# Kernel optimization log

Hardware: AMD Instinct MI355X
Metric: run time of the kernel (lower is better)

## Reference

```python
import jax, jax.numpy as jnp
import numpy as np

D = 8
W = 256
NUM_FREQS = 10
NUM_FREQS_VIEWS = 4
SKIPS = (4,)
PE_DIM = 3 + 2 * 3 * NUM_FREQS        # 63
VE_DIM = 3 + 2 * 3 * NUM_FREQS_VIEWS  # 27
N_RAYS, N_SAMPLES = 4096, 64


def embed(x, num_freqs):
    # torch order: [x, sin(x*f0), cos(x*f0), sin(x*f1), cos(x*f1), ...]
    freqs = (2.0 ** jnp.arange(num_freqs)).astype(x.dtype)
    xf = x[..., None, :] * freqs[:, None]              # [..., F, 3]
    sc = jnp.stack([jnp.sin(xf), jnp.cos(xf)], axis=-2)  # [..., F, 2, 3]
    return jnp.concatenate([x, sc.reshape(*x.shape[:-1], num_freqs * 6)], -1)


def setup_inputs() -> dict:
    key = jax.random.key(0)
    ks = iter(jax.random.split(key, 32))
    inp = {}
    inp["input_pts"] = jax.random.normal(next(ks), (N_RAYS, N_SAMPLES, 3), jnp.float32)
    inp["input_views"] = jax.random.normal(next(ks), (N_RAYS, 3), jnp.float32)
    # pts MLP: layer 5 (index 5) takes W + PE_DIM due to skip after layer 4
    in_dims = [PE_DIM] + [(W + PE_DIM) if i in SKIPS else W for i in range(D - 1)]
    for i, d in enumerate(in_dims):
        inp[f"pts_w{i}"] = jax.random.normal(next(ks), (d, W), jnp.float32) / np.sqrt(d).astype(np.float32)
        inp[f"pts_b{i}"] = jnp.zeros((W,), jnp.float32)
    inp["views_w"] = jax.random.normal(next(ks), (VE_DIM + W, W // 2), jnp.float32) / np.sqrt(VE_DIM + W).astype(np.float32)
    inp["views_b"] = jnp.zeros((W // 2,), jnp.float32)
    inp["feat_w"] = jax.random.normal(next(ks), (W, W), jnp.float32) / np.sqrt(W).astype(np.float32)
    inp["feat_b"] = jnp.zeros((W,), jnp.float32)
    inp["alpha_w"] = jax.random.normal(next(ks), (W, 1), jnp.float32) / np.sqrt(W).astype(np.float32)
    inp["alpha_b"] = jnp.zeros((1,), jnp.float32)
    inp["rgb_w"] = jax.random.normal(next(ks), (W // 2, 3), jnp.float32) / np.sqrt(W // 2).astype(np.float32)
    inp["rgb_b"] = jnp.zeros((3,), jnp.float32)
    return inp


def reference(input_pts, input_views,
              pts_w0, pts_b0, pts_w1, pts_b1, pts_w2, pts_b2, pts_w3, pts_b3,
              pts_w4, pts_b4, pts_w5, pts_b5, pts_w6, pts_b6, pts_w7, pts_b7,
              views_w, views_b, feat_w, feat_b, alpha_w, alpha_b, rgb_w, rgb_b):
    pts_ws = [pts_w0, pts_w1, pts_w2, pts_w3, pts_w4, pts_w5, pts_w6, pts_w7]
    pts_bs = [pts_b0, pts_b1, pts_b2, pts_b3, pts_b4, pts_b5, pts_b6, pts_b7]
    R, S = input_pts.shape[0], input_pts.shape[1]
    ep = embed(input_pts, NUM_FREQS).reshape(-1, PE_DIM)            # [R*S, 63]
    ev = embed(input_views, NUM_FREQS_VIEWS)                        # [R, 27]
    ev = jnp.broadcast_to(ev[:, None, :], (R, S, VE_DIM)).reshape(-1, VE_DIM)
    h = ep
    for i in range(D):
        h = jax.nn.relu(h @ pts_ws[i] + pts_bs[i])
        if i in SKIPS:
            h = jnp.concatenate([ep, h], -1)
    alpha = h @ alpha_w + alpha_b                                    # [R*S, 1]
    feature = h @ feat_w + feat_b                                    # [R*S, W]
    h2 = jax.nn.relu(jnp.concatenate([feature, ev], -1) @ views_w + views_b)
    rgb = h2 @ rgb_w + rgb_b                                         # [R*S, 3]
    return jnp.concatenate([rgb, alpha], -1).reshape(R, S, 4)
```

## Files before the change

### kernel.cpp

```cpp
#include <hip/hip_runtime.h>

typedef _Float16 h16;
typedef __attribute__((ext_vector_type(8))) _Float16 half8;
typedef __attribute__((ext_vector_type(4))) _Float16 half4;
typedef __attribute__((ext_vector_type(4))) float f32x4;
typedef __attribute__((ext_vector_type(16))) float f32x16;

constexpr size_t OFF_P0 = 0;
constexpr size_t OFF_P1 = 16384;
constexpr size_t OFF_P2 = 81920;
constexpr size_t OFF_P3 = 147456;
constexpr size_t OFF_P4 = 212992;
constexpr size_t OFF_P5 = 278528;
constexpr size_t OFF_P6 = 360448;
constexpr size_t OFF_P7 = 425984;
constexpr size_t OFF_FEAT = 491520;
constexpr size_t OFF_VIEWS = 557056;

__device__ __forceinline__ f32x16 mfma32(half8 a, half8 b, f32x16 c) {
  return __builtin_amdgcn_mfma_f32_32x32x16_f16(a, b, c, 0, 0, 0);
}
__device__ __forceinline__ half8 ldfrag(const h16* __restrict__ base, int frag, int l) {
  return *(const half8*)(base + (size_t)frag * 512 + (size_t)l * 8);
}
__device__ __forceinline__ half8 ldsfrag(const h16* __restrict__ base, int frag, int l) {
  return *(const half8*)(base + frag * 512 + l * 8);
}

__global__ void convw_kernel(const float* __restrict__ src, h16* __restrict__ dst,
                             int Ksrc, int N, int Kp, int p, int npad) {
  int t = blockIdx.x * 256 + threadIdx.x;
  int nfrags = (Kp >> 4) * (N >> 5);
  int frag = t >> 6;
  if (frag >= nfrags) return;
  int l = t & 63;
  int ntiles = N >> 5;
  int kt = frag / ntiles;
  int nt = frag - kt * ntiles;
  int col = nt * 32 + (l & 31);
  int kbase = kt * 16 + (l >> 5) * 8;
  half8 v;
#pragma unroll
  for (int j = 0; j < 8; ++j) {
    int k = kbase + j;
    float x = 0.f;
    if (k < p) {
      x = src[(size_t)k * N + col];
    } else if (k >= p + npad) {
      int r = k - npad;
      if (r < Ksrc) x = src[(size_t)r * N + col];
    }
    v[j] = (h16)x;
  }
  *(half8*)(dst + (size_t)frag * 512 + (size_t)l * 8) = v;
}

struct Params {
  const float* pts;
  const float* views;
  const h16* wf;
  const float* pb[8];
  const float* views_b;
  const float* feat_b;
  const float* alpha_w;
  const float* alpha_b;
  const float* rgb_w;
  const float* rgb_b;
  float* out;
};

template <bool RELU>
__device__ __forceinline__ void epiW(h16* __restrict__ Y, const f32x16& A,
                                     int rt, int ct, const float* __restrict__ bias,
                                     int lr, int lh) {
#pragma unroll
  for (int g = 0; g < 4; ++g) {
    int col0 = ct * 32 + g * 8 + lh * 4;
    f32x4 bv = *(const f32x4*)(bias + col0);
    half4 pk;
#pragma unroll
    for (int i = 0; i < 4; ++i) {
      float v = A[g * 4 + i] + bv[i];
      if (RELU) v = fmaxf(v, 0.f);
      pk[i] = (h16)v;
    }
    *(half4*)(Y + (rt * 16 + ct * 2 + (g >> 1)) * 512 + ((g & 1) * 32 + lr) * 8 + lh * 4) = pk;
  }
}

__device__ __forceinline__ float embed_col(int c, float x0, float x1, float x2) {
  if (c < 3) return c == 0 ? x0 : (c == 1 ? x1 : x2);
  if (c >= 63) return 0.f;
  int t = c - 3;
  int f = t / 6, rem = t - f * 6;
  int d = rem >= 3 ? rem - 3 : rem;
  float x = (d == 0 ? x0 : (d == 1 ? x1 : x2)) * (float)(1 << f);
  return (rem < 3) ? sinf(x) : cosf(x);
}

template <bool RELU, bool EXTEP, int WKT0>
__device__ __forceinline__ void layerF(h16* __restrict__ h, const h16* __restrict__ ep,
                                       const h16* __restrict__ wcur,
                                       const float* __restrict__ bias,
                                       int w, int l, int lr, int lh) {
  f32x16 a0 = (f32x16)0.f, a1 = (f32x16)0.f;
#pragma unroll
  for (int kt = 0; kt < 16; ++kt) {
    half8 x0 = ldsfrag(h, kt, l);
    half8 x1 = ldsfrag(h, 16 + kt, l);
    half8 b = ldfrag(wcur, (WKT0 + kt) * 8 + w, l);
    a0 = mfma32(b, x0, a0);
    a1 = mfma32(b, x1, a1);
  }
  if (EXTEP) {
#pragma unroll
    for (int j = 0; j < 4; ++j) {
      half8 x0 = ldsfrag(ep, j, l);
      half8 x1 = ldsfrag(ep, 4 + j, l);
      half8 b = ldfrag(wcur, j * 8 + w, l);
      a0 = mfma32(b, x0, a0);
      a1 = mfma32(b, x1, a1);
    }
  }
  __syncthreads();
  epiW<RELU>(h, a0, 0, w, bias, lr, lh);
  epiW<RELU>(h, a1, 1, w, bias, lr, lh);
  __syncthreads();
}

__global__ __launch_bounds__(512, 6) void nerf_kernel(Params P) {
  __shared__ __align__(16) h16 h[32 * 512];
  __shared__ __align__(16) h16 ep[8 * 512];
  __shared__ __align__(16) h16 evp[32];
  __shared__ float alpha_s[64];

  const int tid = threadIdx.x;
  const int w = tid >> 6, l = tid & 63;
  const int lr = l & 31, lh = l >> 5;
  const int ray = blockIdx.x;
  const h16* wf = P.wf;

  {
    const int s = tid >> 3, q = tid & 7;
    const float* ps = P.pts + ((size_t)ray * 64 + s) * 3;
    const float x0 = ps[0], x1 = ps[1], x2 = ps[2];
    half8 v;
#pragma unroll
    for (int j = 0; j < 8; ++j)
      v[j] = (h16)embed_col(q * 8 + j, x0, x1, x2);
    *(half8*)(ep + ((s >> 5) * 4 + (q >> 1)) * 512 + ((s & 31) + 32 * (q & 1)) * 8) = v;
  }
  if (tid < 32) {
    const int idx = tid;
    float v = 0.f;
    if (idx < 27) {
      if (idx < 3) {
        v = P.views[(size_t)ray * 3 + idx];
      } else {
        const int f = (idx - 3) / 6, rem = (idx - 3) % 6, d = rem % 3;
        const float x = P.views[(size_t)ray * 3 + d] * (float)(1 << f);
        v = (rem < 3) ? sinf(x) : cosf(x);
      }
    }
    evp[idx] = (h16)v;
  }
  __syncthreads();

  {
    f32x16 a0 = (f32x16)0.f, a1 = (f32x16)0.f;
#pragma unroll
    for (int kt = 0; kt < 4; ++kt) {
      half8 x0 = ldsfrag(ep, kt, l);
      half8 x1 = ldsfrag(ep, 4 + kt, l);
      half8 b = ldfrag(wf + OFF_P0, kt * 8 + w, l);
      a0 = mfma32(b, x0, a0);
      a1 = mfma32(b, x1, a1);
    }
    epiW<true>(h, a0, 0, w, P.pb[0], lr, lh);
    epiW<true>(h, a1, 1, w, P.pb[0], lr, lh);
    __syncthreads();
  }

  layerF<true, false, 0>(h, ep, wf + OFF_P1, P.pb[1], w, l, lr, lh);
  layerF<true, false, 0>(h, ep, wf + OFF_P2, P.pb[2], w, l, lr, lh);
  layerF<true, false, 0>(h, ep, wf + OFF_P3, P.pb[3], w, l, lr, lh);
  layerF<true, false, 0>(h, ep, wf + OFF_P4, P.pb[4], w, l, lr, lh);
  layerF<true, true, 4>(h, ep, wf + OFF_P5, P.pb[5], w, l, lr, lh);
  layerF<true, false, 0>(h, ep, wf + OFF_P6, P.pb[6], w, l, lr, lh);
  layerF<true, false, 0>(h, ep, wf + OFF_P7, P.pb[7], w, l, lr, lh);

  {
    const int s = tid >> 3, q = tid & 7;
    float sum = 0.f;
#pragma unroll
    for (int j = 0; j < 4; ++j) {
      int k0 = q * 32 + j * 8;
      half8 hv = *(const half8*)(h + ((s >> 5) * 16 + (k0 >> 4)) * 512 +
                                 ((s & 31) + 32 * ((k0 >> 3) & 1)) * 8);
      f32x4 w0 = *(const f32x4*)(P.alpha_w + k0);
      f32x4 w1 = *(const f32x4*)(P.alpha_w + k0 + 4);
      sum += (float)hv[0] * w0[0] + (float)hv[1] * w0[1] + (float)hv[2] * w0[2] + (float)hv[3] * w0[3];
      sum += (float)hv[4] * w1[0] + (float)hv[5] * w1[1] + (float)hv[6] * w1[2] + (float)hv[7] * w1[3];
    }
    sum += __shfl_xor(sum, 1);
    sum += __shfl_xor(sum, 2);
    sum += __shfl_xor(sum, 4);
    if (q == 0) alpha_s[s] = sum + P.alpha_b[0];
  }

  layerF<false, false, 0>(h, ep, wf + OFF_FEAT, P.feat_b, w, l, lr, lh);

  {
    const int rt = w >> 2, ct = w & 3;
    const h16* wV = wf + OFF_VIEWS;
    f32x16 acc = (f32x16)0.f;
#pragma unroll
    for (int kt = 0; kt < 16; ++kt) {
      half8 x = ldsfrag(h, rt * 16 + kt, l);
      half8 b = ldfrag(wV, kt * 4 + ct, l);
      acc = mfma32(b, x, acc);
    }
#pragma unroll
    for (int kt = 16; kt < 18; ++kt) {
      half8 x = *(const half8*)(evp + (kt - 16) * 16 + lh * 8);
      half8 b = ldfrag(wV, kt * 4 + ct, l);
      acc = mfma32(b, x, acc);
    }
    __syncthreads();
    epiW<true>(h, acc, rt, ct, P.views_b, lr, lh);
    __syncthreads();
  }

  {
    const int s = tid >> 3, q = tid & 7;
    float r0 = 0.f, r1 = 0.f, r2 = 0.f;
#pragma unroll
    for (int j = 0; j < 2; ++j) {
      int k0 = q * 16 + j * 8;
      half8 hv = *(const half8*)(h + ((s >> 5) * 16 + (k0 >> 4)) * 512 +
                                 ((s & 31) + 32 * ((k0 >> 3) & 1)) * 8);
#pragma unroll
      for (int i = 0; i < 8; ++i) {
        const float f = (float)hv[i];
        r0 += f * P.rgb_w[(k0 + i) * 3 + 0];
        r1 += f * P.rgb_w[(k0 + i) * 3 + 1];
        r2 += f * P.rgb_w[(k0 + i) * 3 + 2];
      }
    }
    r0 += __shfl_xor(r0, 1); r0 += __shfl_xor(r0, 2); r0 += __shfl_xor(r0, 4);
    r1 += __shfl_xor(r1, 1); r1 += __shfl_xor(r1, 2); r1 += __shfl_xor(r1, 4);
    r2 += __shfl_xor(r2, 1); r2 += __shfl_xor(r2, 2); r2 += __shfl_xor(r2, 4);
    if (q == 0) {
      float4 o;
      o.x = r0 + P.rgb_b[0];
      o.y = r1 + P.rgb_b[1];
      o.z = r2 + P.rgb_b[2];
      o.w = alpha_s[s];
      *(float4*)(P.out + ((size_t)ray * 64 + s) * 4) = o;
    }
  }
}

extern "C" void kernel_launch(void* const* d_in, const int* in_sizes, int n_in,
                              void* d_out, int out_size, void* d_ws, size_t ws_size,
                              hipStream_t stream) {
  h16* wsw = (h16*)d_ws;
  auto conv = [&](int idx, int Ksrc, int N, int Kp, int p, int npad, size_t off) {
    int nfrags = (Kp / 16) * (N / 32);
    int total = nfrags * 64;
    convw_kernel<<<(total + 255) / 256, 256, 0, stream>>>(
        (const float*)d_in[idx], wsw + off, Ksrc, N, Kp, p, npad);
  };
  conv(2, 63, 256, 64, 63, 1, OFF_P0);
  conv(4, 256, 256, 256, 256, 0, OFF_P1);
  conv(6, 256, 256, 256, 256, 0, OFF_P2);
  conv(8, 256, 256, 256, 256, 0, OFF_P3);
  conv(10, 256, 256, 256, 256, 0, OFF_P4);
  conv(12, 319, 256, 320, 63, 1, OFF_P5);
  conv(14, 256, 256, 256, 256, 0, OFF_P6);
  conv(16, 256, 256, 256, 256, 0, OFF_P7);
  conv(20, 256, 256, 256, 256, 0, OFF_FEAT);
  conv(18, 283, 128, 288, 283, 5, OFF_VIEWS);

  Params P;
  P.pts = (const float*)d_in[0];
  P.views = (const float*)d_in[1];
  P.wf = wsw;
  for (int i = 0; i < 8; ++i) P.pb[i] = (const float*)d_in[3 + 2 * i];
  P.views_b = (const float*)d_in[19];
  P.feat_b = (const float*)d_in[21];
  P.alpha_w = (const float*)d_in[22];
  P.alpha_b = (const float*)d_in[23];
  P.rgb_w = (const float*)d_in[24];
  P.rgb_b = (const float*)d_in[25];
  P.out = (float*)d_out;

  nerf_kernel<<<4096, 512, 0, stream>>>(P);
}
```

Before: 385.5 us.

## Software-pipeline weight fragment loads across layers with a 4-deep register ring

Weight fragments are now prefetched from global memory into a 4-entry register ring buffer four k-steps ahead, and the prefetch carries over into the next layer's first fragments, so global load latency overlaps with MFMA work across layer boundaries. The skip layer is restructured so the ep fragments come first in one unified loop. The occupancy hint in launch bounds is lowered from 6 to 4 blocks per CU to leave room for the extra live registers, which may reduce latency hiding between waves. An extra barrier is added after layer 0.

```diff
diff --git a/kernel.cpp b/kernel.cpp
--- a/kernel.cpp
+++ b/kernel.cpp
@@ -98,29 +98,32 @@
   return (rem < 3) ? sinf(x) : cosf(x);
 }
 
-template <bool RELU, bool EXTEP, int WKT0>
+template <int KT, bool EXTEP, bool RELU>
 __device__ __forceinline__ void layerF(h16* __restrict__ h, const h16* __restrict__ ep,
                                        const h16* __restrict__ wcur,
+                                       const h16* __restrict__ wnextp, int nstride,
                                        const float* __restrict__ bias,
+                                       half8 (&wr)[4],
                                        int w, int l, int lr, int lh) {
   f32x16 a0 = (f32x16)0.f, a1 = (f32x16)0.f;
 #pragma unroll
-  for (int kt = 0; kt < 16; ++kt) {
-    half8 x0 = ldsfrag(h, kt, l);
-    half8 x1 = ldsfrag(h, 16 + kt, l);
-    half8 b = ldfrag(wcur, (WKT0 + kt) * 8 + w, l);
+  for (int i = 0; i < KT; ++i) {
+    half8 x0, x1;
+    if (EXTEP && i < 4) {
+      x0 = ldsfrag(ep, i, l);
+      x1 = ldsfrag(ep, 4 + i, l);
+    } else {
+      const int kt = EXTEP ? i - 4 : i;
+      x0 = ldsfrag(h, kt, l);
+      x1 = ldsfrag(h, 16 + kt, l);
+    }
+    half8 b = wr[i & 3];
+    if (i + 4 < KT)
+      wr[i & 3] = ldfrag(wcur, (i + 4) * 8 + w, l);
+    else
+      wr[i & 3] = ldfrag(wnextp, (i + 4 - KT) * nstride, l);
     a0 = mfma32(b, x0, a0);
     a1 = mfma32(b, x1, a1);
-  }
-  if (EXTEP) {
-#pragma unroll
-    for (int j = 0; j < 4; ++j) {
-      half8 x0 = ldsfrag(ep, j, l);
-      half8 x1 = ldsfrag(ep, 4 + j, l);
-      half8 b = ldfrag(wcur, j * 8 + w, l);
-      a0 = mfma32(b, x0, a0);
-      a1 = mfma32(b, x1, a1);
-    }
   }
   __syncthreads();
   epiW<RELU>(h, a0, 0, w, bias, lr, lh);
@@ -128,7 +131,7 @@
   __syncthreads();
 }
 
-__global__ __launch_bounds__(512, 6) void nerf_kernel(Params P) {
+__global__ __launch_bounds__(512, 4) void nerf_kernel(Params P) {
   __shared__ __align__(16) h16 h[32 * 512];
   __shared__ __align__(16) h16 ep[8 * 512];
   __shared__ __align__(16) h16 evp[32];
@@ -139,6 +142,10 @@
   const int lr = l & 31, lh = l >> 5;
   const int ray = blockIdx.x;
   const h16* wf = P.wf;
+
+  half8 wr[4];
+#pragma unroll
+  for (int j = 0; j < 4; ++j) wr[j] = ldfrag(wf + OFF_P0, j * 8 + w, l);
 
   {
     const int s = tid >> 3, q = tid & 7;
@@ -169,25 +176,27 @@
   {
     f32x16 a0 = (f32x16)0.f, a1 = (f32x16)0.f;
 #pragma unroll
-    for (int kt = 0; kt < 4; ++kt) {
-      half8 x0 = ldsfrag(ep, kt, l);
-      half8 x1 = ldsfrag(ep, 4 + kt, l);
-      half8 b = ldfrag(wf + OFF_P0, kt * 8 + w, l);
+    for (int i = 0; i < 4; ++i) {
+      half8 x0 = ldsfrag(ep, i, l);
+      half8 x1 = ldsfrag(ep, 4 + i, l);
+      half8 b = wr[i & 3];
+      wr[i & 3] = ldfrag(wf + OFF_P1, i * 8 + w, l);
       a0 = mfma32(b, x0, a0);
       a1 = mfma32(b, x1, a1);
     }
+    __syncthreads();
     epiW<true>(h, a0, 0, w, P.pb[0], lr, lh);
     epiW<true>(h, a1, 1, w, P.pb[0], lr, lh);
     __syncthreads();
   }
 
-  layerF<true, false, 0>(h, ep, wf + OFF_P1, P.pb[1], w, l, lr, lh);
-  layerF<true, false, 0>(h, ep, wf + OFF_P2, P.pb[2], w, l, lr, lh);
-  layerF<true, false, 0>(h, ep, wf + OFF_P3, P.pb[3], w, l, lr, lh);
-  layerF<true, false, 0>(h, ep, wf + OFF_P4, P.pb[4], w, l, lr, lh);
-  layerF<true, true, 4>(h, ep, wf + OFF_P5, P.pb[5], w, l, lr, lh);
-  layerF<true, false, 0>(h, ep, wf + OFF_P6, P.pb[6], w, l, lr, lh);
-  layerF<true, false, 0>(h, ep, wf + OFF_P7, P.pb[7], w, l, lr, lh);
+  layerF<16, false, true>(h, ep, wf + OFF_P1, wf + OFF_P2 + (size_t)w * 512, 8, P.pb[1], wr, w, l, lr, lh);
+  layerF<16, false, true>(h, ep, wf + OFF_P2, wf + OFF_P3 + (size_t)w * 512, 8, P.pb[2], wr, w, l, lr, lh);
+  layerF<16, false, true>(h, ep, wf + OFF_P3, wf + OFF_P4 + (size_t)w * 512, 8, P.pb[3], wr, w, l, lr, lh);
+  layerF<16, false, true>(h, ep, wf + OFF_P4, wf + OFF_P5 + (size_t)w * 512, 8, P.pb[4], wr, w, l, lr, lh);
+  layerF<20, true,  true>(h, ep, wf + OFF_P5, wf + OFF_P6 + (size_t)w * 512, 8, P.pb[5], wr, w, l, lr, lh);
+  layerF<16, false, true>(h, ep, wf + OFF_P6, wf + OFF_P7 + (size_t)w * 512, 8, P.pb[6], wr, w, l, lr, lh);
+  layerF<16, false, true>(h, ep, wf + OFF_P7, wf + OFF_FEAT + (size_t)w * 512, 8, P.pb[7], wr, w, l, lr, lh);
 
   {
     const int s = tid >> 3, q = tid & 7;
@@ -208,22 +217,19 @@
     if (q == 0) alpha_s[s] = sum + P.alpha_b[0];
   }
 
-  layerF<false, false, 0>(h, ep, wf + OFF_FEAT, P.feat_b, w, l, lr, lh);
+  layerF<16, false, false>(h, ep, wf + OFF_FEAT, wf + OFF_VIEWS + (size_t)(w & 3) * 512, 4, P.feat_b, wr, w, l, lr, lh);
 
   {
     const int rt = w >> 2, ct = w & 3;
     const h16* wV = wf + OFF_VIEWS;
     f32x16 acc = (f32x16)0.f;
 #pragma unroll
-    for (int kt = 0; kt < 16; ++kt) {
-      half8 x = ldsfrag(h, rt * 16 + kt, l);
-      half8 b = ldfrag(wV, kt * 4 + ct, l);
-      acc = mfma32(b, x, acc);
-    }
-#pragma unroll
-    for (int kt = 16; kt < 18; ++kt) {
-      half8 x = *(const half8*)(evp + (kt - 16) * 16 + lh * 8);
-      half8 b = ldfrag(wV, kt * 4 + ct, l);
+    for (int i = 0; i < 18; ++i) {
+      half8 x;
+      if (i < 16) x = ldsfrag(h, rt * 16 + i, l);
+      else x = *(const half8*)(evp + (i - 16) * 16 + lh * 8);
+      half8 b = wr[i & 3];
+      if (i + 4 < 18) wr[i & 3] = ldfrag(wV, (i + 4) * 4 + ct, l);
       acc = mfma32(b, x, acc);
     }
     __syncthreads();
```

New measurement: 370.0 us. 4.0% less time.
